# Kernel tuning notes

Hardware: AMD Instinct MI355X
Metric: run time of the kernel (lower is better)

Reference implementation:

```python
import jax, jax.numpy as jnp
import numpy as np

B, C, G, K, S, P, R = 4, 256, 16, 7, 1, 3, 4
H = W = 56


def setup_inputs() -> dict:
    key = jax.random.key(0)
    k1, k2, k3 = jax.random.split(key, 3)
    x = jax.random.normal(k1, (B, C, H, W), jnp.float32)
    reduce_w = jax.random.normal(k2, (C // R, C), jnp.float32) * 0.05
    reduce_b = jnp.zeros((C // R,), jnp.float32)
    span_w = jax.random.normal(k3, (K * K * G, C // R), jnp.float32) * 0.05
    span_b = jnp.zeros((K * K * G,), jnp.float32)
    return {"x": x, "reduce_w": reduce_w, "reduce_b": reduce_b,
            "span_w": span_w, "span_b": span_b}


def reference(x, reduce_w, reduce_b, span_w, span_b):
    b, c, h_in, w_in = x.shape
    Ho = (h_in + 2 * P - K) // S + 1
    Wo = (w_in + 2 * P - K) // S + 1
    # im2col patches, channel ordering (C, kh, kw) — matches torch.nn.Unfold
    patches = jax.lax.conv_general_dilated_patches(
        x, (K, K), (S, S), [(P, P), (P, P)])  # (B, C*K*K, Ho, Wo)
    patches = patches.reshape(b, G, c // G, K * K, Ho, Wo)
    # kernel generation branch: AvgPool(s) (identity for s=1) -> 1x1 reduce -> 1x1 span
    if S > 1:
        xk = jax.lax.reduce_window(x, 0.0, jax.lax.add,
                                   (1, 1, S, S), (1, 1, S, S), 'VALID') / (S * S)
    else:
        xk = x
    h = jnp.einsum('bchw,oc->bohw', xk, reduce_w) + reduce_b[None, :, None, None]
    kern = jnp.einsum('bchw,oc->bohw', h, span_w) + span_b[None, :, None, None]
    kern = kern.reshape(b, G, 1, K * K, Ho, Wo)
    # dynamic per-pixel depthwise-style multiply-reduce over the K*K window
    out = (kern * patches).sum(axis=3)  # (B, G, C//G, Ho, Wo)
    return out.reshape(b, c, Ho, Wo)
```

## Files before the change

### kernel.cpp

```cpp
#include <hip/hip_runtime.h>
#include <hip/hip_fp16.h>
#include <stdint.h>

#define HH   56
#define WW   56
#define HWP  3136
#define CC   256
#define GG   16
#define CGR  16
#define KT   7
#define KK   49
#define RCP  32
#define TH   2
#define XROW 32
#define XPL  260

typedef _Float16 h2_t   __attribute__((ext_vector_type(2)));
typedef __fp16   fp16x2 __attribute__((ext_vector_type(2)));
typedef _Float16 v8h    __attribute__((ext_vector_type(8)));
typedef float    v4f    __attribute__((ext_vector_type(4)));
union pk32 { uint32_t u; h2_t h; __half2 hh; fp16x2 f; };
union frag { uint32_t u[4]; v8h h; };

static __device__ __forceinline__ uint32_t pkrtz(float a, float b) {
    pk32 p; p.f = __builtin_amdgcn_cvt_pkrtz(a, b); return p.u;
}

static __device__ __forceinline__ frag pack_afrag(const float* rowp, int quad) {
    frag a;
    const float4 p0 = *(const float4*)&rowp[quad * 8];
    const float4 p1 = *(const float4*)&rowp[quad * 8 + 4];
    a.u[0] = pkrtz(p0.x, p0.y); a.u[1] = pkrtz(p0.z, p0.w);
    a.u[2] = pkrtz(p1.x, p1.y); a.u[3] = pkrtz(p1.z, p1.w);
    return a;
}

__global__ __launch_bounds__(256)
void gemm1_mfma(const float* __restrict__ rw, const float* __restrict__ rb,
                const float* __restrict__ x, uint32_t* __restrict__ h2)
{
    const int b = blockIdx.z, px0 = blockIdx.x * 32;
    const int t = threadIdx.x;
    const int wave = t >> 6, lane = t & 63, quad = lane >> 4, n16 = lane & 15;

    __shared__ __align__(16) uint32_t ldsB[2][8 * 128];

    const int px = t & 31;
    const int q4 = t >> 5;
    const float* xb = x + (size_t)b * CC * HWP + px0 + px;

    float r[4][8];
#pragma unroll
    for (int k = 0; k < 4; ++k)
#pragma unroll
        for (int cc = 0; cc < 8; ++cc)
            r[k][cc] = xb[(size_t)(k * 64 + q4 * 8 + cc) * HWP];

    const float* rwr = rw + (size_t)(wave * 16 + n16) * CC;
    frag af0[4], af1[4];
#pragma unroll
    for (int k = 0; k < 4; ++k) {
        af0[k] = pack_afrag(rwr + k * 64, quad);
        af1[k] = pack_afrag(rwr + k * 64 + 32, quad);
    }

    {
        uint4 w;
        w.x = pkrtz(r[0][0], r[0][1]); w.y = pkrtz(r[0][2], r[0][3]);
        w.z = pkrtz(r[0][4], r[0][5]); w.w = pkrtz(r[0][6], r[0][7]);
        *(uint4*)&ldsB[0][q4 * 128 + px * 4] = w;
    }
    __syncthreads();

    v4f acc[2];
    acc[0] = v4f{0.f,0.f,0.f,0.f}; acc[1] = v4f{0.f,0.f,0.f,0.f};
#pragma unroll
    for (int k = 0; k < 4; ++k) {
        if (k < 3) {
            uint4 w;
            w.x = pkrtz(r[k+1][0], r[k+1][1]); w.y = pkrtz(r[k+1][2], r[k+1][3]);
            w.z = pkrtz(r[k+1][4], r[k+1][5]); w.w = pkrtz(r[k+1][6], r[k+1][7]);
            *(uint4*)&ldsB[(k + 1) & 1][q4 * 128 + px * 4] = w;
        }
        const uint32_t* B = ldsB[k & 1];
#pragma unroll
        for (int nt = 0; nt < 2; ++nt) {
            frag b0, b1;
            *(uint4*)b0.u = *(const uint4*)&B[quad * 128 + (nt * 16 + n16) * 4];
            *(uint4*)b1.u = *(const uint4*)&B[(4 + quad) * 128 + (nt * 16 + n16) * 4];
            acc[nt] = __builtin_amdgcn_mfma_f32_16x16x32_f16(af0[k].h, b0.h, acc[nt], 0, 0, 0);
            acc[nt] = __builtin_amdgcn_mfma_f32_16x16x32_f16(af1[k].h, b1.h, acc[nt], 0, 0, 0);
        }
        __syncthreads();
    }
    uint32_t* hb = h2 + (size_t)b * RCP * HWP + px0;
#pragma unroll
    for (int nt = 0; nt < 2; ++nt)
#pragma unroll
        for (int pr = 0; pr < 2; ++pr) {
            const int m0 = wave * 16 + quad * 4 + 2 * pr;
            hb[(size_t)(wave * 8 + quad * 2 + pr) * HWP + nt * 16 + n16] =
                pkrtz(acc[nt][2 * pr] + rb[m0], acc[nt][2 * pr + 1] + rb[m0 + 1]);
        }
}

__global__ __launch_bounds__(256, 4)
void invol_fused(const float* __restrict__ x, const uint32_t* __restrict__ h2,
                 const float* __restrict__ sw, const float* __restrict__ sb,
                 float* __restrict__ out)
{
    const int h0 = blockIdx.x * TH, g = blockIdx.y, b = blockIdx.z;

    __shared__ __align__(16) uint32_t sXh[16 * XPL];
    __shared__ __align__(16) uint32_t U[8 * 448];

    const int t = threadIdx.x;
    const int wave = t >> 6, lane = t & 63, quad = lane >> 4, n16 = lane & 15;

    const int mt0 = wave * 16 + n16;
    const int mtap = mt0 > 48 ? 48 : mt0;
    const float* swr = sw + (size_t)(g * KK + mtap) * 64;
    const frag a0 = pack_afrag(swr, quad);
    const frag a1 = pack_afrag(swr + 32, quad);

    float bvv[4];
#pragma unroll
    for (int reg = 0; reg < 4; ++reg) {
        const int tp = wave * 16 + quad * 4 + reg;
        bvv[reg] = (tp < KK) ? sb[g * KK + tp] : 0.f;
    }

    {
        const uint32_t* hb = h2 + (size_t)b * RCP * HWP + h0 * WW;
#pragma unroll
        for (int k = 0; k < 4; ++k) {
            const int i = t + 256 * k;
            if (i < 896) {
                const int px = i % 112, q4 = i / 112;
                uint4 w;
                w.x = hb[(size_t)(q4 * 4 + 0) * HWP + px];
                w.y = hb[(size_t)(q4 * 4 + 1) * HWP + px];
                w.z = hb[(size_t)(q4 * 4 + 2) * HWP + px];
                w.w = hb[(size_t)(q4 * 4 + 3) * HWP + px];
                *(uint4*)&U[q4 * 448 + px * 4] = w;
            }
        }
    }

    {
        const int ch = t >> 4, rr = (t >> 1) & 7, side = t & 1;
        uint2 z; z.x = 0; z.y = 0;
        *(uint2*)&sXh[ch * XPL + rr * XROW + (side ? 30 : 0)] = z;
    }

    {
        const float* xb = x + (size_t)(b * CC + g * CGR) * HWP;
#pragma unroll
        for (int k = 0; k < 7; ++k) {
            const int i = t + 256 * k;
            const int w4 = i % 14, rr = (i / 14) % 8, ch = i / 112;
            const int hh = h0 - 3 + rr;
            float4 v = make_float4(0.f, 0.f, 0.f, 0.f);
            if (hh >= 0 && hh < HH)
                v = *(const float4*)&xb[(size_t)ch * HWP + hh * WW + 4 * w4];
            uint2 p; p.x = pkrtz(v.x, v.y); p.y = pkrtz(v.z, v.w);
            *(uint2*)&sXh[ch * XPL + rr * XROW + 2 + 2 * w4] = p;
        }
    }
    __syncthreads();

    v4f acc[7];
#pragma unroll
    for (int nt = 0; nt < 7; ++nt) acc[nt] = v4f{0.f,0.f,0.f,0.f};
#pragma unroll
    for (int nt = 0; nt < 7; ++nt) {
        const int pxm = (nt * 16 + n16) * 4;
        frag b0, b1;
        *(uint4*)b0.u = *(const uint4*)&U[quad * 448 + pxm];
        *(uint4*)b1.u = *(const uint4*)&U[(4 + quad) * 448 + pxm];
        acc[nt] = __builtin_amdgcn_mfma_f32_16x16x32_f16(a0.h, b0.h, acc[nt], 0, 0, 0);
        acc[nt] = __builtin_amdgcn_mfma_f32_16x16x32_f16(a1.h, b1.h, acc[nt], 0, 0, 0);
    }
    __syncthreads();

    {
        _Float16* sK = (_Float16*)U;
#pragma unroll
        for (int nt = 0; nt < 7; ++nt) {
            const int px = nt * 16 + n16;
#pragma unroll
            for (int reg = 0; reg < 4; ++reg) {
                const int tp = wave * 16 + quad * 4 + reg;
                if (tp < KK) sK[tp * 112 + px] = (_Float16)(acc[nt][reg] + bvv[reg]);
            }
        }
    }
    __syncthreads();

    if (t < 224) {
        const int ch = t & 15, q = t >> 4, r = q & 1, wq = q >> 1;
        const uint32_t* xpl = &sXh[ch * XPL + 4 * wq];
        float o0=0,o1=0,o2=0,o3=0,o4=0,o5=0,o6=0,o7=0;
#pragma unroll
        for (int kh = 0; kh < KT; ++kh) {
            const int rr = r + kh;
            uint32_t E[8];
            *(uint4*)&E[0] = *(const uint4*)&xpl[rr * XROW];
            *(uint4*)&E[4] = *(const uint4*)&xpl[rr * XROW + 4];
            uint32_t O[7];
#pragma unroll
            for (int j = 0; j < 7; ++j) O[j] = __builtin_amdgcn_alignbit(E[j + 1], E[j], 16);
            pk32 va0, va1, va2, va3;
            va0.u = va1.u = va2.u = va3.u = 0;
            const uint32_t* kq = &U[(kh * KT) * 56 + r * 28 + 4 * wq];
#pragma unroll
            for (int kw = 0; kw < KT; ++kw) {
                const uint4 kk = *(const uint4*)&kq[kw * 56];
                pk32 k0, k1, k2, k3; k0.u = kk.x; k1.u = kk.y; k2.u = kk.z; k3.u = kk.w;
                pk32 s0, s1, s2, s3;
                if (kw & 1) {
                    const int e = (kw + 1) >> 1;
                    s0.u = E[e]; s1.u = E[e + 1]; s2.u = E[e + 2]; s3.u = E[e + 3];
                } else {
                    const int oI = kw >> 1;
                    s0.u = O[oI]; s1.u = O[oI + 1]; s2.u = O[oI + 2]; s3.u = O[oI + 3];
                }
                va0.hh = __hfma2(k0.hh, s0.hh, va0.hh);
                va1.hh = __hfma2(k1.hh, s1.hh, va1.hh);
                va2.hh = __hfma2(k2.hh, s2.hh, va2.hh);
                va3.hh = __hfma2(k3.hh, s3.hh, va3.hh);
            }
            const float2 f0 = __half22float2(va0.hh); o0 += f0.x; o1 += f0.y;
            const float2 f1 = __half22float2(va1.hh); o2 += f1.x; o3 += f1.y;
            const float2 f2 = __half22float2(va2.hh); o4 += f2.x; o5 += f2.y;
            const float2 f3 = __half22float2(va3.hh); o6 += f3.x; o7 += f3.y;
        }
        float* op = out + (size_t)(b * CC + g * CGR + ch) * HWP + (h0 + r) * WW + 8 * wq;
        *(float4*)&op[0] = make_float4(o0, o1, o2, o3);
        *(float4*)&op[4] = make_float4(o4, o5, o6, o7);
    }
}

extern "C" void kernel_launch(void* const* d_in, const int* in_sizes, int n_in,
                              void* d_out, int out_size, void* d_ws, size_t ws_size,
                              hipStream_t stream)
{
    const float* x  = (const float*)d_in[0];
    const float* rw = (const float*)d_in[1];
    const float* rb = (const float*)d_in[2];
    const float* sw = (const float*)d_in[3];
    const float* sb = (const float*)d_in[4];
    float* out  = (float*)d_out;

    uint32_t* h2 = (uint32_t*)d_ws;

    gemm1_mfma<<<dim3(HWP / 32, 1, 4), 256, 0, stream>>>(rw, rb, x, h2);
    invol_fused<<<dim3(HH / TH, GG, 4), 256, 0, stream>>>(x, h2, sw, sb, out);
}
```

Before: 95.77 us.

## Store reduced features in MFMA-fragment-swizzled blocks and load B directly from global

The first kernel now transposes its output through LDS and writes the reduced activations in 16-pixel blocks laid out exactly as the MFMA B-fragments need them. The second kernel then reads B fragments straight from global memory with 16-byte loads, with no LDS staging. This removes one LDS round trip and one barrier, shrinks LDS use, and raises the launch-bounds occupancy hint from 4 to 5. In exchange, the first kernel gains an extra LDS transpose and barrier, and the MFMA operands now wait on global-memory latency.

```diff
diff --git a/kernel.cpp b/kernel.cpp
--- a/kernel.cpp
+++ b/kernel.cpp
@@ -10,10 +10,11 @@
 #define CGR  16
 #define KT   7
 #define KK   49
-#define RCP  32
 #define TH   2
 #define XROW 32
 #define XPL  260
+#define PBLK 512
+#define NPB  196
 
 typedef _Float16 h2_t   __attribute__((ext_vector_type(2)));
 typedef __fp16   fp16x2 __attribute__((ext_vector_type(2)));
@@ -37,13 +38,13 @@
 
 __global__ __launch_bounds__(256)
 void gemm1_mfma(const float* __restrict__ rw, const float* __restrict__ rb,
-                const float* __restrict__ x, uint32_t* __restrict__ h2)
+                const float* __restrict__ x, uint32_t* __restrict__ h2s)
 {
     const int b = blockIdx.z, px0 = blockIdx.x * 32;
     const int t = threadIdx.x;
     const int wave = t >> 6, lane = t & 63, quad = lane >> 4, n16 = lane & 15;
 
-    __shared__ __align__(16) uint32_t ldsB[2][8 * 128];
+    __shared__ __align__(16) uint32_t ldsB[2][1024];
 
     const int px = t & 31;
     const int q4 = t >> 5;
@@ -93,26 +94,40 @@
         }
         __syncthreads();
     }
-    uint32_t* hb = h2 + (size_t)b * RCP * HWP + px0;
+
+    uint32_t* ldsT = &ldsB[0][0];
 #pragma unroll
     for (int nt = 0; nt < 2; ++nt)
 #pragma unroll
         for (int pr = 0; pr < 2; ++pr) {
-            const int m0 = wave * 16 + quad * 4 + 2 * pr;
-            hb[(size_t)(wave * 8 + quad * 2 + pr) * HWP + nt * 16 + n16] =
-                pkrtz(acc[nt][2 * pr] + rb[m0], acc[nt][2 * pr + 1] + rb[m0 + 1]);
-        }
-}
-
-__global__ __launch_bounds__(256, 4)
-void invol_fused(const float* __restrict__ x, const uint32_t* __restrict__ h2,
+            const int cp = wave * 8 + quad * 2 + pr;
+            ldsT[cp * 33 + nt * 16 + n16] =
+                pkrtz(acc[nt][2 * pr] + rb[2 * cp], acc[nt][2 * pr + 1] + rb[2 * cp + 1]);
+        }
+    __syncthreads();
+    {
+        const int oq4 = t >> 5, px32 = t & 31;
+        uint4 w;
+        w.x = ldsT[(oq4 * 4 + 0) * 33 + px32];
+        w.y = ldsT[(oq4 * 4 + 1) * 33 + px32];
+        w.z = ldsT[(oq4 * 4 + 2) * 33 + px32];
+        w.w = ldsT[(oq4 * 4 + 3) * 33 + px32];
+        uint32_t* hp = h2s + (size_t)b * NPB * PBLK
+                     + (size_t)(blockIdx.x * 2 + (px32 >> 4)) * PBLK
+                     + oq4 * 64 + (px32 & 15) * 4;
+        *(uint4*)hp = w;
+    }
+}
+
+__global__ __launch_bounds__(256, 5)
+void invol_fused(const float* __restrict__ x, const uint32_t* __restrict__ h2s,
                  const float* __restrict__ sw, const float* __restrict__ sb,
                  float* __restrict__ out)
 {
     const int h0 = blockIdx.x * TH, g = blockIdx.y, b = blockIdx.z;
 
     __shared__ __align__(16) uint32_t sXh[16 * XPL];
-    __shared__ __align__(16) uint32_t U[8 * 448];
+    __shared__ __align__(16) uint32_t sK[KK * 56];
 
     const int t = threadIdx.x;
     const int wave = t >> 6, lane = t & 63, quad = lane >> 4, n16 = lane & 15;
@@ -131,28 +146,10 @@
     }
 
     {
-        const uint32_t* hb = h2 + (size_t)b * RCP * HWP + h0 * WW;
-#pragma unroll
-        for (int k = 0; k < 4; ++k) {
-            const int i = t + 256 * k;
-            if (i < 896) {
-                const int px = i % 112, q4 = i / 112;
-                uint4 w;
-                w.x = hb[(size_t)(q4 * 4 + 0) * HWP + px];
-                w.y = hb[(size_t)(q4 * 4 + 1) * HWP + px];
-                w.z = hb[(size_t)(q4 * 4 + 2) * HWP + px];
-                w.w = hb[(size_t)(q4 * 4 + 3) * HWP + px];
-                *(uint4*)&U[q4 * 448 + px * 4] = w;
-            }
-        }
-    }
-
-    {
         const int ch = t >> 4, rr = (t >> 1) & 7, side = t & 1;
         uint2 z; z.x = 0; z.y = 0;
         *(uint2*)&sXh[ch * XPL + rr * XROW + (side ? 30 : 0)] = z;
     }
-
     {
         const float* xb = x + (size_t)(b * CC + g * CGR) * HWP;
 #pragma unroll
@@ -167,31 +164,29 @@
             *(uint2*)&sXh[ch * XPL + rr * XROW + 2 + 2 * w4] = p;
         }
     }
-    __syncthreads();
-
-    v4f acc[7];
-#pragma unroll
-    for (int nt = 0; nt < 7; ++nt) acc[nt] = v4f{0.f,0.f,0.f,0.f};
-#pragma unroll
-    for (int nt = 0; nt < 7; ++nt) {
-        const int pxm = (nt * 16 + n16) * 4;
-        frag b0, b1;
-        *(uint4*)b0.u = *(const uint4*)&U[quad * 448 + pxm];
-        *(uint4*)b1.u = *(const uint4*)&U[(4 + quad) * 448 + pxm];
-        acc[nt] = __builtin_amdgcn_mfma_f32_16x16x32_f16(a0.h, b0.h, acc[nt], 0, 0, 0);
-        acc[nt] = __builtin_amdgcn_mfma_f32_16x16x32_f16(a1.h, b1.h, acc[nt], 0, 0, 0);
-    }
-    __syncthreads();
-
-    {
-        _Float16* sK = (_Float16*)U;
+
+    {
+        const uint32_t* hb = h2s + (size_t)b * NPB * PBLK + (size_t)(blockIdx.x * 7) * PBLK;
+        v4f acc[7];
+#pragma unroll
+        for (int nt = 0; nt < 7; ++nt) acc[nt] = v4f{0.f,0.f,0.f,0.f};
+#pragma unroll
+        for (int nt = 0; nt < 7; ++nt) {
+            const uint32_t* pb = hb + nt * PBLK + n16 * 4;
+            frag b0, b1;
+            *(uint4*)b0.u = *(const uint4*)&pb[quad * 64];
+            *(uint4*)b1.u = *(const uint4*)&pb[(4 + quad) * 64];
+            acc[nt] = __builtin_amdgcn_mfma_f32_16x16x32_f16(a0.h, b0.h, acc[nt], 0, 0, 0);
+            acc[nt] = __builtin_amdgcn_mfma_f32_16x16x32_f16(a1.h, b1.h, acc[nt], 0, 0, 0);
+        }
+        _Float16* sKh = (_Float16*)sK;
 #pragma unroll
         for (int nt = 0; nt < 7; ++nt) {
             const int px = nt * 16 + n16;
 #pragma unroll
             for (int reg = 0; reg < 4; ++reg) {
                 const int tp = wave * 16 + quad * 4 + reg;
-                if (tp < KK) sK[tp * 112 + px] = (_Float16)(acc[nt][reg] + bvv[reg]);
+                if (tp < KK) sKh[tp * 112 + px] = (_Float16)(acc[nt][reg] + bvv[reg]);
             }
         }
     }
@@ -212,7 +207,7 @@
             for (int j = 0; j < 7; ++j) O[j] = __builtin_amdgcn_alignbit(E[j + 1], E[j], 16);
             pk32 va0, va1, va2, va3;
             va0.u = va1.u = va2.u = va3.u = 0;
-            const uint32_t* kq = &U[(kh * KT) * 56 + r * 28 + 4 * wq];
+            const uint32_t* kq = &sK[(kh * KT) * 56 + r * 28 + 4 * wq];
 #pragma unroll
             for (int kw = 0; kw < KT; ++kw) {
                 const uint4 kk = *(const uint4*)&kq[kw * 56];
@@ -252,8 +247,8 @@
     const float* sb = (const float*)d_in[4];
     float* out  = (float*)d_out;
 
-    uint32_t* h2 = (uint32_t*)d_ws;
-
-    gemm1_mfma<<<dim3(HWP / 32, 1, 4), 256, 0, stream>>>(rw, rb, x, h2);
-    invol_fused<<<dim3(HH / TH, GG, 4), 256, 0, stream>>>(x, h2, sw, sb, out);
-}
+    uint32_t* h2s = (uint32_t*)d_ws;
+
+    gemm1_mfma<<<dim3(HWP / 32, 1, 4), 256, 0, stream>>>(rw, rb, x, h2s);
+    invol_fused<<<dim3(HH / TH, GG, 4), 256, 0, stream>>>(x, h2s, sw, sb, out);
+}
```

After: 95.15 us. Within noise of the previous version (-0.7%).
